# Kernel tuning notes

Measured on AMD Instinct MI355X. Metric: run time of the kernel, lower is better.

Reference implementation:

```python
import jax, jax.numpy as jnp
import numpy as np

D_MODEL = 1024
H = 16
D_K = D_MODEL // H
B = 2
S = 2048
NEG = -1e10


def setup_inputs() -> dict:
    key = jax.random.key(0)
    ks = jax.random.split(key, 12)
    sc = 1.0 / np.sqrt(D_MODEL)
    inp = {
        "q": jax.random.normal(ks[0], (B, S, D_MODEL), jnp.float32),
        "k": jax.random.normal(ks[1], (B, S, D_MODEL), jnp.float32),
        "v": jax.random.normal(ks[2], (B, S, D_MODEL), jnp.float32),
        # causal mask, broadcast over batch and heads
        "mask": jnp.tril(jnp.ones((S, S), jnp.int32))[None, None, :, :],
        "w_q": jax.random.normal(ks[3], (D_MODEL, D_MODEL), jnp.float32) * sc,
        "b_q": jax.random.normal(ks[4], (D_MODEL,), jnp.float32) * sc,
        "w_k": jax.random.normal(ks[5], (D_MODEL, D_MODEL), jnp.float32) * sc,
        "b_k": jax.random.normal(ks[6], (D_MODEL,), jnp.float32) * sc,
        "w_v": jax.random.normal(ks[7], (D_MODEL, D_MODEL), jnp.float32) * sc,
        "b_v": jax.random.normal(ks[8], (D_MODEL,), jnp.float32) * sc,
        "w_o": jax.random.normal(ks[9], (D_MODEL, D_MODEL), jnp.float32) * sc,
        "b_o": jax.random.normal(ks[10], (D_MODEL,), jnp.float32) * sc,
    }
    return inp


def _split_heads(x):
    # [B, S, D] -> [B, H, S, d_k]
    b, s, _ = x.shape
    return x.reshape(b, s, H, D_K).transpose(0, 2, 1, 3)


def reference(q, k, v, mask, w_q, b_q, w_k, b_k, w_v, b_v, w_o, b_o):
    # Linear projections (torch Linear: x @ W.T + b)
    qh = _split_heads(q @ w_q.T + b_q)
    kh = _split_heads(k @ w_k.T + b_k)
    vh = _split_heads(v @ w_v.T + b_v)
    scale = 1.0 / jnp.sqrt(jnp.asarray(D_K, qh.dtype))
    scores = jnp.einsum("bhqd,bhkd->bhqk", qh, kh) * scale
    scores = jnp.where(mask == 0, jnp.asarray(NEG, scores.dtype), scores)
    attn = jax.nn.softmax(scores, axis=-1)  # dropout=0.0 -> identity
    x = jnp.einsum("bhqk,bhkd->bhqd", attn, vh)
    x = x.transpose(0, 2, 1, 3).reshape(q.shape[0], -1, H * D_K)
    out = x @ w_o.T + b_o
    return (out, attn)
```

## Files before the change

### kernel.cpp

```cpp
#include <hip/hip_runtime.h>
#include <hip/hip_bf16.h>

typedef unsigned short u16;
typedef unsigned int u32;
typedef __attribute__((ext_vector_type(8))) short bf16x8;
typedef __attribute__((ext_vector_type(4))) float f32x4;

#define SEQ 2048
#define DM 1024
#define NH 16
#define DKK 64
#define NB 2

__device__ __forceinline__ u16 f2bf(float f) {
  union { float f; u32 u; } x; x.f = f;
  u32 r = x.u + 0x7FFFu + ((x.u >> 16) & 1u);
  return (u16)(r >> 16);
}

__device__ __forceinline__ void gl_lds16(const void* g, void* l) {
  __builtin_amdgcn_global_load_lds(
      (const __attribute__((address_space(1))) u32*)g,
      (__attribute__((address_space(3))) u32*)l, 16, 0, 0);
}

#define MFMA16(a, b, c) __builtin_amdgcn_mfma_f32_16x16x32_bf16(a, b, c, 0, 0, 0)
#define VMCNT0() asm volatile("s_waitcnt vmcnt(0)" ::: "memory")
#define SCHEDB() __builtin_amdgcn_sched_barrier(0)

__global__ __launch_bounds__(256) void cvt3(const float* __restrict__ i0,
                                            const float* __restrict__ i1,
                                            const float* __restrict__ i2,
                                            u16* o0, u16* o1, u16* o2, int n4) {
  const float* in = (blockIdx.y == 0) ? i0 : (blockIdx.y == 1) ? i1 : i2;
  u16* out = (blockIdx.y == 0) ? o0 : (blockIdx.y == 1) ? o1 : o2;
  int i = blockIdx.x * 256 + threadIdx.x;
  if (i >= n4) return;
  float4 v = ((const float4*)in)[i];
  ushort4 o;
  o.x = f2bf(v.x); o.y = f2bf(v.y); o.z = f2bf(v.z); o.w = f2bf(v.w);
  ((ushort4*)out)[i] = o;
}

__global__ __launch_bounds__(256) void cvt4(const float* __restrict__ i0,
                                            const float* __restrict__ i1,
                                            const float* __restrict__ i2,
                                            const float* __restrict__ i3,
                                            u16* o0, u16* o1, u16* o2, u16* o3,
                                            int n4) {
  const float* in = (blockIdx.y == 0) ? i0
                    : (blockIdx.y == 1) ? i1
                    : (blockIdx.y == 2) ? i2 : i3;
  u16* out = (blockIdx.y == 0) ? o0
             : (blockIdx.y == 1) ? o1
             : (blockIdx.y == 2) ? o2 : o3;
  int i = blockIdx.x * 256 + threadIdx.x;
  if (i >= n4) return;
  float4 v = ((const float4*)in)[i];
  ushort4 o;
  o.x = f2bf(v.x); o.y = f2bf(v.y); o.z = f2bf(v.z); o.w = f2bf(v.w);
  ((ushort4*)out)[i] = o;
}

struct ProjArgs {
  const u16* A;
  const u16* W;
  const float* bias;
  u16* Y;
  float scale;
};

__global__ __launch_bounds__(256) void proj_qkv(ProjArgs a0, ProjArgs a1,
                                                ProjArgs a2) {
  ProjArgs pa = (blockIdx.z == 0) ? a0 : (blockIdx.z == 1) ? a1 : a2;
  __shared__ __align__(16) u16 As[2][128 * 32];
  __shared__ __align__(16) u16 Bs[2][128 * 32];
  const int tid = threadIdx.x, lane = tid & 63, w = tid >> 6;
  const int lr = lane & 15, lg = lane >> 4;
  const int wr = w >> 1, wc = w & 1;
  const int r0 = blockIdx.x * 128, c0 = blockIdx.y * 128;
  f32x4 acc[4][4];
#pragma unroll
  for (int i = 0; i < 4; ++i)
#pragma unroll
    for (int j = 0; j < 4; ++j) acc[i][j] = (f32x4){0.f, 0.f, 0.f, 0.f};

  auto stage = [&](int k0, int buf) {
#pragma unroll
    for (int c = 0; c < 2; ++c) {
      int idx = tid + 256 * c;
      int row = idx >> 2, seg = idx & 3;
      gl_lds16(pa.A + (size_t)(r0 + row) * DM + k0 + seg * 8,
               (char*)As[buf] + idx * 16);
      gl_lds16(pa.W + (size_t)(c0 + row) * DM + k0 + seg * 8,
               (char*)Bs[buf] + idx * 16);
    }
  };

  stage(0, 0);
  __syncthreads();
  int buf = 0;
  const int NT = DM / 32;
  for (int t = 0; t < NT; ++t) {
    if (t + 1 < NT) stage((t + 1) * 32, buf ^ 1);
    bf16x8 a[4], b[4];
#pragma unroll
    for (int i = 0; i < 4; ++i) {
      int row = wr * 64 + i * 16 + lr;
      a[i] = *(const bf16x8*)((const char*)As[buf] + row * 64 + lg * 16);
    }
#pragma unroll
    for (int j = 0; j < 4; ++j) {
      int row = wc * 64 + j * 16 + lr;
      b[j] = *(const bf16x8*)((const char*)Bs[buf] + row * 64 + lg * 16);
    }
#pragma unroll
    for (int i = 0; i < 4; ++i)
#pragma unroll
      for (int j = 0; j < 4; ++j) acc[i][j] = MFMA16(a[i], b[j], acc[i][j]);
    __syncthreads();
    buf ^= 1;
  }
#pragma unroll
  for (int i = 0; i < 4; ++i)
#pragma unroll
    for (int j = 0; j < 4; ++j)
#pragma unroll
      for (int rg = 0; rg < 4; ++rg) {
        int row = r0 + wr * 64 + i * 16 + lg * 4 + rg;
        int col = c0 + wc * 64 + j * 16 + lr;
        float v = (acc[i][j][rg] + pa.bias[col]) * pa.scale;
        int bb = row >> 11, s = row & (SEQ - 1), h = col >> 6, d = col & 63;
        pa.Y[((size_t)(bb * NH + h) * SEQ + s) * DKK + d] = f2bf(v);
      }
}

__global__ __launch_bounds__(256) void mm_out(const u16* __restrict__ A,
                                              const u16* __restrict__ W,
                                              const float* __restrict__ bias,
                                              float* __restrict__ Y) {
  __shared__ __align__(16) u16 As[2][128 * 32];
  __shared__ __align__(16) u16 Bs[2][128 * 32];
  const int tid = threadIdx.x, lane = tid & 63, w = tid >> 6;
  const int lr = lane & 15, lg = lane >> 4;
  const int wr = w >> 1, wc = w & 1;
  const int r0 = blockIdx.x * 128, c0 = blockIdx.y * 128;
  f32x4 acc[4][4];
#pragma unroll
  for (int i = 0; i < 4; ++i)
#pragma unroll
    for (int j = 0; j < 4; ++j) acc[i][j] = (f32x4){0.f, 0.f, 0.f, 0.f};

  auto stage = [&](int k0, int buf) {
#pragma unroll
    for (int c = 0; c < 2; ++c) {
      int idx = tid + 256 * c;
      int row = idx >> 2, seg = idx & 3;
      gl_lds16(A + (size_t)(r0 + row) * DM + k0 + seg * 8,
               (char*)As[buf] + idx * 16);
      gl_lds16(W + (size_t)(c0 + row) * DM + k0 + seg * 8,
               (char*)Bs[buf] + idx * 16);
    }
  };

  stage(0, 0);
  __syncthreads();
  int buf = 0;
  const int NT = DM / 32;
  for (int t = 0; t < NT; ++t) {
    if (t + 1 < NT) stage((t + 1) * 32, buf ^ 1);
    bf16x8 a[4], b[4];
#pragma unroll
    for (int i = 0; i < 4; ++i) {
      int row = wr * 64 + i * 16 + lr;
      a[i] = *(const bf16x8*)((const char*)As[buf] + row * 64 + lg * 16);
    }
#pragma unroll
    for (int j = 0; j < 4; ++j) {
      int row = wc * 64 + j * 16 + lr;
      b[j] = *(const bf16x8*)((const char*)Bs[buf] + row * 64 + lg * 16);
    }
#pragma unroll
    for (int i = 0; i < 4; ++i)
#pragma unroll
      for (int j = 0; j < 4; ++j) acc[i][j] = MFMA16(a[i], b[j], acc[i][j]);
    __syncthreads();
    buf ^= 1;
  }
#pragma unroll
  for (int i = 0; i < 4; ++i)
#pragma unroll
    for (int j = 0; j < 4; ++j)
#pragma unroll
      for (int rg = 0; rg < 4; ++rg) {
        int row = r0 + wr * 64 + i * 16 + lg * 4 + rg;
        int col = c0 + wc * 64 + j * 16 + lr;
        Y[(size_t)row * DM + col] = acc[i][j][rg] + bias[col];
      }
}

__global__ __launch_bounds__(256) void transpose_v(const u16* __restrict__ Vh,
                                                   u16* __restrict__ Vt) {
  const int st = blockIdx.x, bh = blockIdx.y;
  const u16* src = Vh + ((size_t)bh * SEQ + st * 64) * DKK;
  u16* dst = Vt + (size_t)bh * DKK * SEQ + st * 64;
  __shared__ u16 T[64][68];
  const int tid = threadIdx.x;
#pragma unroll
  for (int c = 0; c < 4; ++c) {
    int idx = tid + 256 * c;
    int r = idx >> 4, seg = idx & 15;
    ushort4 v = *(const ushort4*)(src + r * 64 + seg * 4);
    *(ushort4*)&T[r][seg * 4] = v;
  }
  __syncthreads();
#pragma unroll
  for (int c = 0; c < 4; ++c) {
    int idx = tid + 256 * c;
    int d = idx >> 4, sseg = idx & 15;
    ushort4 o;
    o.x = T[sseg * 4 + 0][d]; o.y = T[sseg * 4 + 1][d];
    o.z = T[sseg * 4 + 2][d]; o.w = T[sseg * 4 + 3][d];
    *(ushort4*)(dst + (size_t)d * SEQ + sseg * 4) = o;
  }
}

__global__ __launch_bounds__(256) void flash_fwd(const u16* __restrict__ Qh,
                                                 const u16* __restrict__ Kh,
                                                 const u16* __restrict__ Vt,
                                                 u16* __restrict__ X,
                                                 float* __restrict__ linv) {
  const int lin = (int)(blockIdx.y * gridDim.x + blockIdx.x);
  const int nwg = (int)(gridDim.x * gridDim.y);
  const int swz = (lin & 7) * (nwg >> 3) + (lin >> 3);
  const int qi = (int)gridDim.x - 1 - (swz & 15);
  const int bh = swz >> 4;
  const int q0 = qi * 128;
  const u16* Qb = Qh + (size_t)bh * SEQ * DKK;
  const u16* Kb = Kh + (size_t)bh * SEQ * DKK;
  const u16* Vb = Vt + (size_t)bh * DKK * SEQ;
  const int tid = threadIdx.x, lane = tid & 63, w = tid >> 6;
  const int lr = lane & 15, lg = lane >> 4;

  __shared__ __align__(16) u16 Ks[2][64 * 64];
  __shared__ __align__(16) u16 Vs[2][64 * 64];
  __shared__ __align__(16) u16 Ps[4 * 32 * 64];

  bf16x8 frQ[2][2];
#pragma unroll
  for (int ri = 0; ri < 2; ++ri)
#pragma unroll
    for (int kc = 0; kc < 2; ++kc) {
      int r = q0 + w * 32 + ri * 16 + lr;
      frQ[ri][kc] = *(const bf16x8*)(Qb + (size_t)r * DKK + kc * 32 + lg * 8);
    }

  f32x4 accO[2][4];
  float rs[2] = {0.f, 0.f};
#pragma unroll
  for (int ri = 0; ri < 2; ++ri)
#pragma unroll
    for (int ci = 0; ci < 4; ++ci) accO[ri][ci] = (f32x4){0.f, 0.f, 0.f, 0.f};

  const int wmax = q0 + w * 32 + 31;
  const int nkv = (qi + 1) * 2;

  auto stage = [&](int j, int buf) {
    const int kv0 = j * 64;
#pragma unroll
    for (int c = 0; c < 2; ++c) {
      int idx = tid + 256 * c;
      int row = idx >> 3, sq = idx & 7;
      int seg = sq ^ (row & 7);
      gl_lds16(Kb + (size_t)(kv0 + row) * DKK + seg * 8,
               (char*)Ks[buf] + idx * 16);
      gl_lds16(Vb + (size_t)row * SEQ + kv0 + seg * 8,
               (char*)Vs[buf] + idx * 16);
    }
  };

  stage(0, 0);
  VMCNT0();
  __builtin_amdgcn_s_barrier();
  SCHEDB();

  for (int j = 0; j < nkv; ++j) {
    const int buf = j & 1;
    const int kv0 = j * 64;
    if (j + 1 < nkv) stage(j + 1, buf ^ 1);

    if (kv0 <= wmax) {
      __builtin_amdgcn_s_setprio(1);
      f32x4 sf[4][2];
#pragma unroll
      for (int ci = 0; ci < 4; ++ci) {
        bf16x8 aK[2];
#pragma unroll
        for (int kc = 0; kc < 2; ++kc) {
          int row = ci * 16 + lr;
          int q = (kc * 4 + lg) ^ (row & 7);
          aK[kc] = *(const bf16x8*)((const char*)Ks[buf] + row * 128 + q * 16);
        }
#pragma unroll
        for (int ri = 0; ri < 2; ++ri) {
          f32x4 a = (f32x4){0.f, 0.f, 0.f, 0.f};
          a = MFMA16(aK[0], frQ[ri][0], a);
          a = MFMA16(aK[1], frQ[ri][1], a);
          sf[ci][ri] = a;
        }
      }
#pragma unroll
      for (int ri = 0; ri < 2; ++ri) {
        const int qglob = q0 + w * 32 + ri * 16 + lr;
        const int qlrow = ri * 16 + lr;
#pragma unroll
        for (int ci = 0; ci < 4; ++ci) {
          float p[4];
#pragma unroll
          for (int rg = 0; rg < 4; ++rg) {
            int kvglob = kv0 + ci * 16 + lg * 4 + rg;
            p[rg] = (kvglob <= qglob) ? __expf(sf[ci][ri][rg]) : 0.f;
          }
          rs[ri] += (p[0] + p[1]) + (p[2] + p[3]);
          u32 lo = (u32)f2bf(p[0]) | ((u32)f2bf(p[1]) << 16);
          u32 hi = (u32)f2bf(p[2]) | ((u32)f2bf(p[3]) << 16);
          int c16 = (ci * 2 + (lg >> 1)) ^ (lr & 7);
          char* dst = (char*)Ps + w * 4096 + qlrow * 128 + c16 * 16 +
                      (lg & 1) * 8;
          *(uint2*)dst = (uint2){lo, hi};
        }
      }
#pragma unroll
      for (int kvc = 0; kvc < 2; ++kvc) {
        bf16x8 aP[2];
#pragma unroll
        for (int ri = 0; ri < 2; ++ri) {
          int qlrow = ri * 16 + lr;
          int c16 = (kvc * 4 + lg) ^ (lr & 7);
          aP[ri] = *(const bf16x8*)((const char*)Ps + w * 4096 + qlrow * 128 +
                                    c16 * 16);
        }
#pragma unroll
        for (int ci = 0; ci < 4; ++ci) {
          int row = ci * 16 + lr;
          int q2 = (kvc * 4 + lg) ^ (row & 7);
          bf16x8 bV =
              *(const bf16x8*)((const char*)Vs[buf] + row * 128 + q2 * 16);
#pragma unroll
          for (int ri = 0; ri < 2; ++ri)
            accO[ri][ci] = MFMA16(aP[ri], bV, accO[ri][ci]);
        }
      }
      __builtin_amdgcn_s_setprio(0);
    }
    VMCNT0();
    __builtin_amdgcn_s_barrier();
    SCHEDB();
  }

  const int b = bh >> 4, h = bh & (NH - 1);
  float vinv[2];
#pragma unroll
  for (int ri = 0; ri < 2; ++ri) {
    float v = rs[ri];
    v += __shfl_xor(v, 16);
    v += __shfl_xor(v, 32);
    float iv = 1.f / v;
    vinv[ri] = iv;
    int qglob = q0 + w * 32 + ri * 16 + lr;
    if (lg == 0) linv[(size_t)bh * SEQ + qglob] = iv;
  }
  float inv_[2][4];
#pragma unroll
  for (int ri = 0; ri < 2; ++ri)
#pragma unroll
    for (int rg = 0; rg < 4; ++rg)
      inv_[ri][rg] = __shfl(vinv[ri], lg * 4 + rg);

#pragma unroll
  for (int ri = 0; ri < 2; ++ri)
#pragma unroll
    for (int ci = 0; ci < 4; ++ci)
#pragma unroll
      for (int rg = 0; rg < 4; ++rg) {
        int srow = q0 + w * 32 + ri * 16 + lg * 4 + rg;
        int col = h * DKK + ci * 16 + lr;
        X[((size_t)(b * SEQ + srow)) * DM + col] =
            f2bf(accO[ri][ci][rg] * inv_[ri][rg]);
      }
}

__global__ __launch_bounds__(256) void attn_mat(const u16* __restrict__ Qh,
                                                const u16* __restrict__ Kh,
                                                const float* __restrict__ linv,
                                                float* __restrict__ attn) {
  const int rt = blockIdx.x, ct = blockIdx.y, bh = blockIdx.z;
  float* out = attn + (size_t)bh * SEQ * SEQ;
  const int tid = threadIdx.x;
  if (ct > rt) {
    float4 z = {0.f, 0.f, 0.f, 0.f};
#pragma unroll
    for (int c = 0; c < 4; ++c) {
      int idx = tid + 256 * c;
      int row = idx >> 4, c4 = idx & 15;
      *(float4*)(out + (size_t)(rt * 64 + row) * SEQ + ct * 64 + c4 * 4) = z;
    }
    return;
  }
  const u16* Qb = Qh + (size_t)bh * SEQ * DKK;
  const u16* Kb = Kh + (size_t)bh * SEQ * DKK;
  __shared__ __align__(16) u16 Qs[64 * 64];
  __shared__ __align__(16) u16 Ks2[64 * 64];
  const int lane = tid & 63, w = tid >> 6, lr = lane & 15, lg = lane >> 4;
#pragma unroll
  for (int c = 0; c < 2; ++c) {
    int idx = tid + 256 * c;
    int row = idx >> 3, sq = idx & 7, seg = sq ^ (row & 7);
    gl_lds16(Qb + (size_t)(rt * 64 + row) * DKK + seg * 8,
             (char*)Qs + idx * 16);
    gl_lds16(Kb + (size_t)(ct * 64 + row) * DKK + seg * 8,
             (char*)Ks2 + idx * 16);
  }
  __syncthreads();
  bf16x8 aQ[2];
#pragma unroll
  for (int kc = 0; kc < 2; ++kc) {
    int row = w * 16 + lr;
    int q = (kc * 4 + lg) ^ (row & 7);
    aQ[kc] = *(const bf16x8*)((const char*)Qs + row * 128 + q * 16);
  }
  float lrow[4];
#pragma unroll
  for (int rg = 0; rg < 4; ++rg)
    lrow[rg] = linv[(size_t)bh * SEQ + rt * 64 + w * 16 + lg * 4 + rg];
  const bool full = (ct < rt);
#pragma unroll
  for (int ci = 0; ci < 4; ++ci) {
    bf16x8 bK[2];
#pragma unroll
    for (int kc = 0; kc < 2; ++kc) {
      int row = ci * 16 + lr;
      int q = (kc * 4 + lg) ^ (row & 7);
      bK[kc] = *(const bf16x8*)((const char*)Ks2 + row * 128 + q * 16);
    }
    f32x4 a = (f32x4){0.f, 0.f, 0.f, 0.f};
    a = MFMA16(aQ[0], bK[0], a);
    a = MFMA16(aQ[1], bK[1], a);
#pragma unroll
    for (int rg = 0; rg < 4; ++rg) {
      int row = rt * 64 + w * 16 + lg * 4 + rg;
      int col = ct * 64 + ci * 16 + lr;
      float v = (full || col <= row) ? __expf(a[rg]) * lrow[rg] : 0.f;
      out[(size_t)row * SEQ + col] = v;
    }
  }
}

extern "C" void kernel_launch(void* const* d_in, const int* in_sizes, int n_in,
                              void* d_out, int out_size, void* d_ws,
                              size_t ws_size, hipStream_t stream) {
  const float* q = (const float*)d_in[0];
  const float* k = (const float*)d_in[1];
  const float* v = (const float*)d_in[2];
  const float* w_q = (const float*)d_in[4];
  const float* b_q = (const float*)d_in[5];
  const float* w_k = (const float*)d_in[6];
  const float* b_k = (const float*)d_in[7];
  const float* w_v = (const float*)d_in[8];
  const float* b_v = (const float*)d_in[9];
  const float* w_o = (const float*)d_in[10];
  const float* b_o = (const float*)d_in[11];

  float* out = (float*)d_out;
  float* attn = out + (size_t)NB * SEQ * DM;

  const size_t MB = 1u << 20;
  char* ws = (char*)d_ws;
  u16* qb = (u16*)(ws);
  u16* kb = (u16*)(ws + 8 * MB);
  u16* vb = (u16*)(ws + 16 * MB);
  u16* Qh = (u16*)(ws + 24 * MB);
  u16* Kh = (u16*)(ws + 32 * MB);
  u16* Vh = (u16*)(ws + 40 * MB);
  u16* wqb = (u16*)(ws + 48 * MB);
  u16* wkb = (u16*)(ws + 50 * MB);
  u16* wvb = (u16*)(ws + 52 * MB);
  u16* wob = (u16*)(ws + 54 * MB);
  float* linv = (float*)(ws + 56 * MB);
  u16* Vt = qb;
  u16* X = vb;

  dim3 blk(256);
  const int n4_qkv = NB * SEQ * DM / 4;
  const int n4_w = DM * DM / 4;
  cvt3<<<dim3((n4_qkv + 255) / 256, 3), blk, 0, stream>>>(q, k, v, qb, kb, vb,
                                                          n4_qkv);
  cvt4<<<dim3((n4_w + 255) / 256, 4), blk, 0, stream>>>(
      w_q, w_k, w_v, w_o, wqb, wkb, wvb, wob, n4_w);

  ProjArgs aq = {qb, wqb, b_q, Qh, 0.125f};
  ProjArgs ak = {kb, wkb, b_k, Kh, 1.0f};
  ProjArgs av = {vb, wvb, b_v, Vh, 1.0f};
  proj_qkv<<<dim3(NB * SEQ / 128, DM / 128, 3), blk, 0, stream>>>(aq, ak, av);

  transpose_v<<<dim3(SEQ / 64, NB * NH), blk, 0, stream>>>(Vh, Vt);

  flash_fwd<<<dim3(SEQ / 128, NB * NH), blk, 0, stream>>>(Qh, Kh, Vt, X, linv);

  mm_out<<<dim3(NB * SEQ / 128, DM / 128), blk, 0, stream>>>(X, wob, b_o, out);

  attn_mat<<<dim3(SEQ / 64, SEQ / 64, NB * NH), blk, 0, stream>>>(Qh, Kh, linv,
                                                                  attn);
}
```

Before: 285.1 us.

## Merge conversion kernels and restructure attn_mat to loop over key tiles per row block

The two fp32-to-bf16 conversion launches are merged into one launch over seven tensors, with the smaller weight tensors exiting early by bound check. The attention-matrix kernel now uses one block per 64-row query tile per head instead of one per 64x64 tile. Each block keeps its Q fragments in registers, loops over key tiles reading K directly from global memory without LDS, swaps the MFMA operands so each lane writes a contiguous float4, and zero-fills the masked tiles itself. This saves launches and Q reloads and gives wider stores, but the grid becomes much smaller and work is triangularly imbalanced across blocks, since early row tiles do little compute.

New measurement: 428.3 us. 1.5x slower.

```diff
diff --git a/kernel.cpp b/kernel.cpp
--- a/kernel.cpp
+++ b/kernel.cpp
@@ -28,32 +28,17 @@
 #define VMCNT0() asm volatile("s_waitcnt vmcnt(0)" ::: "memory")
 #define SCHEDB() __builtin_amdgcn_sched_barrier(0)
 
-__global__ __launch_bounds__(256) void cvt3(const float* __restrict__ i0,
-                                            const float* __restrict__ i1,
-                                            const float* __restrict__ i2,
-                                            u16* o0, u16* o1, u16* o2, int n4) {
-  const float* in = (blockIdx.y == 0) ? i0 : (blockIdx.y == 1) ? i1 : i2;
-  u16* out = (blockIdx.y == 0) ? o0 : (blockIdx.y == 1) ? o1 : o2;
-  int i = blockIdx.x * 256 + threadIdx.x;
-  if (i >= n4) return;
-  float4 v = ((const float4*)in)[i];
-  ushort4 o;
-  o.x = f2bf(v.x); o.y = f2bf(v.y); o.z = f2bf(v.z); o.w = f2bf(v.w);
-  ((ushort4*)out)[i] = o;
-}
-
-__global__ __launch_bounds__(256) void cvt4(const float* __restrict__ i0,
-                                            const float* __restrict__ i1,
-                                            const float* __restrict__ i2,
-                                            const float* __restrict__ i3,
-                                            u16* o0, u16* o1, u16* o2, u16* o3,
-                                            int n4) {
-  const float* in = (blockIdx.y == 0) ? i0
-                    : (blockIdx.y == 1) ? i1
-                    : (blockIdx.y == 2) ? i2 : i3;
-  u16* out = (blockIdx.y == 0) ? o0
-             : (blockIdx.y == 1) ? o1
-             : (blockIdx.y == 2) ? o2 : o3;
+struct CvtArgs {
+  const float* in[7];
+  u16* out[7];
+  int n4[7];
+};
+
+__global__ __launch_bounds__(256) void cvt_all(CvtArgs a) {
+  const int y = blockIdx.y;
+  const float* in = a.in[y];
+  u16* out = a.out[y];
+  const int n4 = a.n4[y];
   int i = blockIdx.x * 256 + threadIdx.x;
   if (i >= n4) return;
   float4 v = ((const float4*)in)[i];
@@ -394,65 +379,68 @@
                                                 const u16* __restrict__ Kh,
                                                 const float* __restrict__ linv,
                                                 float* __restrict__ attn) {
-  const int rt = blockIdx.x, ct = blockIdx.y, bh = blockIdx.z;
-  float* out = attn + (size_t)bh * SEQ * SEQ;
-  const int tid = threadIdx.x;
-  if (ct > rt) {
-    float4 z = {0.f, 0.f, 0.f, 0.f};
-#pragma unroll
-    for (int c = 0; c < 4; ++c) {
-      int idx = tid + 256 * c;
-      int row = idx >> 4, c4 = idx & 15;
-      *(float4*)(out + (size_t)(rt * 64 + row) * SEQ + ct * 64 + c4 * 4) = z;
-    }
-    return;
-  }
+  const int rt = blockIdx.x, bh = blockIdx.y;
   const u16* Qb = Qh + (size_t)bh * SEQ * DKK;
   const u16* Kb = Kh + (size_t)bh * SEQ * DKK;
-  __shared__ __align__(16) u16 Qs[64 * 64];
-  __shared__ __align__(16) u16 Ks2[64 * 64];
-  const int lane = tid & 63, w = tid >> 6, lr = lane & 15, lg = lane >> 4;
-#pragma unroll
-  for (int c = 0; c < 2; ++c) {
-    int idx = tid + 256 * c;
-    int row = idx >> 3, sq = idx & 7, seg = sq ^ (row & 7);
-    gl_lds16(Qb + (size_t)(rt * 64 + row) * DKK + seg * 8,
-             (char*)Qs + idx * 16);
-    gl_lds16(Kb + (size_t)(ct * 64 + row) * DKK + seg * 8,
-             (char*)Ks2 + idx * 16);
-  }
-  __syncthreads();
-  bf16x8 aQ[2];
-#pragma unroll
-  for (int kc = 0; kc < 2; ++kc) {
-    int row = w * 16 + lr;
-    int q = (kc * 4 + lg) ^ (row & 7);
-    aQ[kc] = *(const bf16x8*)((const char*)Qs + row * 128 + q * 16);
-  }
-  float lrow[4];
-#pragma unroll
-  for (int rg = 0; rg < 4; ++rg)
-    lrow[rg] = linv[(size_t)bh * SEQ + rt * 64 + w * 16 + lg * 4 + rg];
-  const bool full = (ct < rt);
-#pragma unroll
-  for (int ci = 0; ci < 4; ++ci) {
-    bf16x8 bK[2];
-#pragma unroll
-    for (int kc = 0; kc < 2; ++kc) {
-      int row = ci * 16 + lr;
-      int q = (kc * 4 + lg) ^ (row & 7);
-      bK[kc] = *(const bf16x8*)((const char*)Ks2 + row * 128 + q * 16);
-    }
-    f32x4 a = (f32x4){0.f, 0.f, 0.f, 0.f};
-    a = MFMA16(aQ[0], bK[0], a);
-    a = MFMA16(aQ[1], bK[1], a);
-#pragma unroll
-    for (int rg = 0; rg < 4; ++rg) {
-      int row = rt * 64 + w * 16 + lg * 4 + rg;
-      int col = ct * 64 + ci * 16 + lr;
-      float v = (full || col <= row) ? __expf(a[rg]) * lrow[rg] : 0.f;
-      out[(size_t)row * SEQ + col] = v;
-    }
+  const int tid = threadIdx.x, lane = tid & 63, w = tid >> 6;
+  const int lr = lane & 15, lg = lane >> 4;
+  const int qrow = rt * 64 + w * 16 + lr;
+
+  bf16x8 frQ[2];
+#pragma unroll
+  for (int kc = 0; kc < 2; ++kc)
+    frQ[kc] = *(const bf16x8*)(Qb + (size_t)qrow * DKK + kc * 32 + lg * 8);
+  const float li = linv[(size_t)bh * SEQ + qrow];
+  float* orow = attn + (size_t)bh * SEQ * SEQ + (size_t)qrow * SEQ;
+
+  for (int ct = 0; ct < rt; ++ct) {
+    const int kv0 = ct * 64;
+#pragma unroll
+    for (int ci = 0; ci < 4; ++ci) {
+      bf16x8 aK[2];
+#pragma unroll
+      for (int kc = 0; kc < 2; ++kc)
+        aK[kc] = *(const bf16x8*)(Kb + (size_t)(kv0 + ci * 16 + lr) * DKK +
+                                  kc * 32 + lg * 8);
+      f32x4 a = (f32x4){0.f, 0.f, 0.f, 0.f};
+      a = MFMA16(aK[0], frQ[0], a);
+      a = MFMA16(aK[1], frQ[1], a);
+      float4 o;
+      o.x = __expf(a[0]) * li;
+      o.y = __expf(a[1]) * li;
+      o.z = __expf(a[2]) * li;
+      o.w = __expf(a[3]) * li;
+      *(float4*)(orow + kv0 + ci * 16 + lg * 4) = o;
+    }
+  }
+  {
+    const int kv0 = rt * 64;
+#pragma unroll
+    for (int ci = 0; ci < 4; ++ci) {
+      bf16x8 aK[2];
+#pragma unroll
+      for (int kc = 0; kc < 2; ++kc)
+        aK[kc] = *(const bf16x8*)(Kb + (size_t)(kv0 + ci * 16 + lr) * DKK +
+                                  kc * 32 + lg * 8);
+      f32x4 a = (f32x4){0.f, 0.f, 0.f, 0.f};
+      a = MFMA16(aK[0], frQ[0], a);
+      a = MFMA16(aK[1], frQ[1], a);
+      float4 o;
+#pragma unroll
+      for (int rg = 0; rg < 4; ++rg) {
+        int kv = kv0 + ci * 16 + lg * 4 + rg;
+        float p = (kv <= qrow) ? __expf(a[rg]) * li : 0.f;
+        ((float*)&o)[rg] = p;
+      }
+      *(float4*)(orow + kv0 + ci * 16 + lg * 4) = o;
+    }
+  }
+  const float4 z = {0.f, 0.f, 0.f, 0.f};
+  for (int ct = rt + 1; ct < SEQ / 64; ++ct) {
+    const int kv0 = ct * 64;
+#pragma unroll
+    for (int ci = 0; ci < 4; ++ci)
+      *(float4*)(orow + kv0 + ci * 16 + lg * 4) = z;
   }
 }
 
@@ -493,10 +481,16 @@
   dim3 blk(256);
   const int n4_qkv = NB * SEQ * DM / 4;
   const int n4_w = DM * DM / 4;
-  cvt3<<<dim3((n4_qkv + 255) / 256, 3), blk, 0, stream>>>(q, k, v, qb, kb, vb,
-                                                          n4_qkv);
-  cvt4<<<dim3((n4_w + 255) / 256, 4), blk, 0, stream>>>(
-      w_q, w_k, w_v, w_o, wqb, wkb, wvb, wob, n4_w);
+
+  CvtArgs ca;
+  ca.in[0] = q;   ca.out[0] = qb;  ca.n4[0] = n4_qkv;
+  ca.in[1] = k;   ca.out[1] = kb;  ca.n4[1] = n4_qkv;
+  ca.in[2] = v;   ca.out[2] = vb;  ca.n4[2] = n4_qkv;
+  ca.in[3] = w_q; ca.out[3] = wqb; ca.n4[3] = n4_w;
+  ca.in[4] = w_k; ca.out[4] = wkb; ca.n4[4] = n4_w;
+  ca.in[5] = w_v; ca.out[5] = wvb; ca.n4[5] = n4_w;
+  ca.in[6] = w_o; ca.out[6] = wob; ca.n4[6] = n4_w;
+  cvt_all<<<dim3((n4_qkv + 255) / 256, 7), blk, 0, stream>>>(ca);
 
   ProjArgs aq = {qb, wqb, b_q, Qh, 0.125f};
   ProjArgs ak = {kb, wkb, b_k, Kh, 1.0f};
@@ -509,6 +503,5 @@
 
   mm_out<<<dim3(NB * SEQ / 128, DM / 128), blk, 0, stream>>>(X, wob, b_o, out);
 
-  attn_mat<<<dim3(SEQ / 64, SEQ / 64, NB * NH), blk, 0, stream>>>(Qh, Kh, linv,
-                                                                  attn);
-}
+  attn_mat<<<dim3(SEQ / 64, NB * NH), blk, 0, stream>>>(Qh, Kh, linv, attn);
+}
```
